# Kernel tuning notes

Measured on AMD Instinct MI355X. Metric: run time of the kernel, lower is better.

Reference implementation:

```python
import jax, jax.numpy as jnp
import numpy as np

B, PLEN, D = 32, 1024, 256


def setup_inputs() -> dict:
    key = jax.random.key(0)
    ks = jax.random.split(key, 8)
    u = lambda k, shape: jax.random.uniform(k, shape, jnp.float32, -0.05, 0.05)
    return {
        "P": jax.random.normal(ks[0], (B, PLEN, D), jnp.float32),
        "w_itr_att": u(ks[1], (3 * D,)),
        "w1": u(ks[2], (2 * D, D)),
        "w2": u(ks[3], (2 * D, D)),
        "w3": u(ks[4], (2 * D, D)),
        "b1": u(ks[5], (D,)),
        "b2": u(ks[6], (D,)),
        "b3": u(ks[7], (D,)),
    }


def reference(P, w_itr_att, w1, w2, w3, b1, b2, b3):
    d = P.shape[-1]
    # alpha(a,b) = w_itr_att . [a ; b ; a*b]; split w into the three d-chunks
    wa, wb, wc = w_itr_att[:d], w_itr_att[d:2 * d], w_itr_att[2 * d:]
    # pairwise score A[b,i,j] = wa.P_i + wb.P_j + wc.(P_i * P_j)
    sa = P @ wa                                   # (b, p)
    sb = P @ wb                                   # (b, p)
    A = sa[:, :, None] + sb[:, None, :] + jnp.einsum('bid,bjd->bij', P * wc, P)
    itr_attn = jnp.einsum('bij,bjd->bid', jax.nn.softmax(A, axis=2), P)
    cat = jnp.concatenate([P, itr_attn], axis=-1)  # (b, p, 2d)
    z = jnp.tanh(cat @ w1 + b1)
    r = jax.nn.sigmoid(cat @ w2 + b2)
    f = jax.nn.sigmoid(cat @ w3 + b3)
    return r * P + f * z
```

## Files before the change

kernel.cpp:

```cpp
#include <hip/hip_runtime.h>
#include <hip/hip_bf16.h>

typedef unsigned short u16;
typedef unsigned int   u32;

using bf16x8 = __attribute__((ext_vector_type(8))) short;
using f32x4  = __attribute__((ext_vector_type(4))) float;

#define NB 32
#define NP 1024
#define ND 256

__device__ __forceinline__ u16 f2bf(float x){
  u32 u = __float_as_uint(x);
  u += 0x7FFFu + ((u >> 16) & 1u);
  return (u16)(u >> 16);
}

__device__ __forceinline__ float bf2f(u16 x){
  return __uint_as_float((u32)x << 16);
}

__device__ __forceinline__ void glds16(const void* g, void* l){
  __builtin_amdgcn_global_load_lds((const __attribute__((address_space(1))) void*)g,
                                   (__attribute__((address_space(3))) void*)l, 16, 0, 0);
}

__global__ void prep_rows(const float* __restrict__ P, const float* __restrict__ wi,
                          u16* __restrict__ Pbf, float* __restrict__ sbv){
  const int row  = blockIdx.x * 4 + (threadIdx.x >> 6);
  const int lane = threadIdx.x & 63;
  const float4 p  = *(const float4*)(P  + (size_t)row * ND + lane * 4);
  const float4 wb = *(const float4*)(wi + ND + lane * 4);
  ushort4 pb;
  pb.x = f2bf(p.x); pb.y = f2bf(p.y); pb.z = f2bf(p.z); pb.w = f2bf(p.w);
  *(ushort4*)(Pbf + (size_t)row * ND + lane * 4) = pb;
  float s = p.x*wb.x + p.y*wb.y + p.z*wb.z + p.w*wb.w;
  #pragma unroll
  for (int m = 1; m < 64; m <<= 1) s += __shfl_xor(s, m, 64);
  if (lane == 0) sbv[row] = s;
}

__global__ void prep_w(const float* __restrict__ w1, const float* __restrict__ w2,
                       const float* __restrict__ w3, u16* __restrict__ Wp){
  const int t = blockIdx.x;
  const float* w = (t < 16) ? w1 : ((t < 32) ? w2 : w3);
  const int tid = threadIdx.x;
  #pragma unroll
  for (int j = 0; j < 4; ++j){
    int item = tid + 256 * j;
    int c = item >> 6, lane = item & 63;
    int ncol = ((t & 15) << 4) + (lane & 15);
    int k0 = 32 * c + 8 * (lane >> 4);
    u16 tmp[8];
    #pragma unroll
    for (int e = 0; e < 8; ++e) tmp[e] = f2bf(w[(size_t)(k0 + e) * 256 + ncol]);
    *(uint4*)(Wp + ((size_t)(t * 16 + c) * 64 + lane) * 8) = *(uint4*)tmp;
  }
}

__global__ void transpose_p(const u16* __restrict__ Pbf, u16* __restrict__ PbfT){
  const int b = blockIdx.z, jt = blockIdx.x, dt = blockIdx.y;
  __shared__ u16 T[64][72];
  const int tid = threadIdx.x;
  #pragma unroll
  for (int it = 0; it < 2; ++it){
    int cc = tid + 256 * it;
    int j = cc >> 3, c8 = cc & 7;
    uint4 v = *(const uint4*)(Pbf + ((size_t)b * NP + jt * 64 + j) * ND + dt * 64 + c8 * 8);
    *(uint4*)&T[j][c8 * 8] = v;
  }
  __syncthreads();
  #pragma unroll
  for (int it = 0; it < 2; ++it){
    int cc = tid + 256 * it;
    int d = cc >> 3, c8 = cc & 7;
    u16 tmp[8];
    #pragma unroll
    for (int k = 0; k < 8; ++k) tmp[k] = T[c8 * 8 + k][d];
    *(uint4*)(PbfT + ((size_t)b * ND + dt * 64 + d) * NP + jt * 64 + c8 * 8) = *(uint4*)tmp;
  }
}

__launch_bounds__(512, 1)
__global__ void attn_kernel(const float* __restrict__ P, const float* __restrict__ wi,
                            const u16* __restrict__ Pbf, const u16* __restrict__ PbfT,
                            const float* __restrict__ sbv, u16* __restrict__ attnb){
  const int p    = blockIdx.x;
  const int bid  = ((p & 7) << 5) | (p >> 3);
  const int b    = bid >> 3;
  const int q0   = (bid & 7) << 7;
  const int tid  = threadIdx.x;
  const int wave = tid >> 6, lane = tid & 63, lo = lane & 15, hi = lane >> 4;

  __shared__ __align__(16) u16 KtA[2][16384];
  __shared__ __align__(16) u16 VtA[2][16384];
  __shared__ __align__(16) u16 Sp[8][16][72];

  bf16x8 qf[8];
  {
    const int qrow = q0 + wave * 16 + lo;
    const float* prow = P  + ((size_t)b * NP + qrow) * ND;
    const float* wcp  = wi + 512;
    #pragma unroll
    for (int c = 0; c < 8; ++c){
      const int d0 = 32 * c + 8 * hi;
      float4 a  = *(const float4*)(prow + d0);
      float4 a2 = *(const float4*)(prow + d0 + 4);
      float4 wa  = *(const float4*)(wcp + d0);
      float4 wa2 = *(const float4*)(wcp + d0 + 4);
      bf16x8 q;
      q[0]=(short)f2bf(a.x*wa.x);  q[1]=(short)f2bf(a.y*wa.y);
      q[2]=(short)f2bf(a.z*wa.z);  q[3]=(short)f2bf(a.w*wa.w);
      q[4]=(short)f2bf(a2.x*wa2.x); q[5]=(short)f2bf(a2.y*wa2.y);
      q[6]=(short)f2bf(a2.z*wa2.z); q[7]=(short)f2bf(a2.w*wa2.w);
      qf[c] = q;
    }
  }

  f32x4 of[16];
  #pragma unroll
  for (int t = 0; t < 16; ++t) of[t] = (f32x4){0.f,0.f,0.f,0.f};
  float mx[4] = {-1e30f,-1e30f,-1e30f,-1e30f};
  float ls[4] = {0.f,0.f,0.f,0.f};

  const u16* kslab = Pbf  + (size_t)b * NP * ND;
  const u16* vslab = PbfT + (size_t)b * ND * NP;

  auto stageKV = [&](int kt, int buf){
    const int kbase = kt * 64;
    char* KtB = (char*)KtA[buf];
    char* VtB = (char*)VtA[buf];
    #pragma unroll
    for (int r = 0; r < 4; ++r){
      int off = r * 8192 + tid * 16;
      int ck  = off >> 10;
      int row = ((off >> 4) & 63) ^ ((ck & 1) << 4);
      glds16((const char*)(kslab + (size_t)(kbase + row) * ND + ck * 8), KtB + off);
    }
    #pragma unroll
    for (int r = 0; r < 4; ++r){
      int off = r * 8192 + tid * 16;
      int c   = off >> 12;
      int d   = ((off >> 4) & 255) ^ ((c & 1) << 4);
      glds16((const char*)(vslab + (size_t)d * NP + kbase + c * 8), VtB + off);
    }
  };

  float sbc[4], sbn[4];
  stageKV(0, 0);
  #pragma unroll
  for (int nt = 0; nt < 4; ++nt) sbc[nt] = sbv[(size_t)b * NP + nt * 16 + lo];
  __syncthreads();

  for (int kt = 0; kt < 16; ++kt){
    const int cur = kt & 1;
    if (kt < 15){
      stageKV(kt + 1, cur ^ 1);
      #pragma unroll
      for (int nt = 0; nt < 4; ++nt)
        sbn[nt] = sbv[(size_t)b * NP + (kt + 1) * 64 + nt * 16 + lo];
    }
    const char* KtB = (const char*)KtA[cur];
    const char* VtB = (const char*)VtA[cur];

    f32x4 s[4];
    #pragma unroll
    for (int nt = 0; nt < 4; ++nt){
      f32x4 acc = (f32x4){0.f,0.f,0.f,0.f};
      #pragma unroll
      for (int c = 0; c < 8; ++c){
        int ck = 4 * c + hi;
        int ad = ck * 1024 + ((((nt << 4) + lo) ^ ((ck & 1) << 4)) << 4);
        bf16x8 kf = *(const bf16x8*)(KtB + ad);
        acc = __builtin_amdgcn_mfma_f32_16x16x32_bf16(qf[c], kf, acc, 0, 0, 0);
      }
      s[nt] = acc;
      float sv = sbc[nt];
      #pragma unroll
      for (int r = 0; r < 4; ++r) s[nt][r] += sv;
    }

    float scale[4];
    #pragma unroll
    for (int r = 0; r < 4; ++r){
      float v = fmaxf(fmaxf(s[0][r], s[1][r]), fmaxf(s[2][r], s[3][r]));
      v = fmaxf(v, __shfl_xor(v, 1, 64));
      v = fmaxf(v, __shfl_xor(v, 2, 64));
      v = fmaxf(v, __shfl_xor(v, 4, 64));
      v = fmaxf(v, __shfl_xor(v, 8, 64));
      float mnew = fmaxf(mx[r], v);
      scale[r] = __expf(mx[r] - mnew);
      mx[r] = mnew;
      float rs = 0.f;
      #pragma unroll
      for (int nt = 0; nt < 4; ++nt){
        float pv = __expf(s[nt][r] - mnew);
        s[nt][r] = pv; rs += pv;
      }
      rs += __shfl_xor(rs, 1, 64);
      rs += __shfl_xor(rs, 2, 64);
      rs += __shfl_xor(rs, 4, 64);
      rs += __shfl_xor(rs, 8, 64);
      ls[r] = ls[r] * scale[r] + rs;
    }
    #pragma unroll
    for (int t = 0; t < 16; ++t){
      #pragma unroll
      for (int r = 0; r < 4; ++r) of[t][r] *= scale[r];
    }
    #pragma unroll
    for (int nt = 0; nt < 4; ++nt)
      #pragma unroll
      for (int r = 0; r < 4; ++r)
        Sp[wave][4 * hi + r][16 * nt + lo] = f2bf(s[nt][r]);

    #pragma unroll
    for (int kk = 0; kk < 2; ++kk){
      bf16x8 pa = *(const bf16x8*)&Sp[wave][lo][32 * kk + 8 * hi];
      int c = 4 * kk + hi;
      int cb = c * 4096, cs = (c & 1) << 4;
      #pragma unroll
      for (int t = 0; t < 16; ++t){
        int ad = cb + ((((t << 4) + lo) ^ cs) << 4);
        bf16x8 vb = *(const bf16x8*)(VtB + ad);
        of[t] = __builtin_amdgcn_mfma_f32_16x16x32_bf16(pa, vb, of[t], 0, 0, 0);
      }
    }
    sbc[0] = sbn[0]; sbc[1] = sbn[1]; sbc[2] = sbn[2]; sbc[3] = sbn[3];
    if (kt < 15) __syncthreads();
  }

  const int qrow = q0 + wave * 16;
  #pragma unroll
  for (int t = 0; t < 16; ++t){
    #pragma unroll
    for (int r = 0; r < 4; ++r){
      float o = of[t][r] / ls[r];
      attnb[((size_t)b * NP + qrow + 4 * hi + r) * ND + 16 * t + lo] = f2bf(o);
    }
  }
}

__launch_bounds__(256, 2)
__global__ void mlp_kernel(const u16* __restrict__ Pbf, const u16* __restrict__ attnb,
                           const u16* __restrict__ Wp,
                           const float* __restrict__ b1, const float* __restrict__ b2,
                           const float* __restrict__ b3, float* __restrict__ out){
  const int p    = blockIdx.x;
  const int swz  = ((p & 7) << 7) | (p >> 3);
  const int mt   = swz >> 2, cg = swz & 3;
  const int tid  = threadIdx.x;
  const int wave = tid >> 6, lane = tid & 63, lo = lane & 15, hi = lane >> 4;
  const int tq   = 4 * cg + wave;
  const int m0   = mt * 128;

  __shared__ __align__(16) u16 Ab[2][128 * 64];

  f32x4 acc[3][8];
  #pragma unroll
  for (int e = 0; e < 3; ++e)
    #pragma unroll
    for (int m = 0; m < 8; ++m) acc[e][m] = (f32x4){0.f,0.f,0.f,0.f};

  auto stage = [&](int s, int buf){
    const u16* xs = (s < 4) ? (Pbf   + (size_t)m0 * ND + s * 64)
                            : (attnb + (size_t)m0 * ND + (s - 4) * 64);
    char* dst = (char*)Ab[buf];
    #pragma unroll
    for (int it = 0; it < 4; ++it){
      int off = it * 4096 + wave * 1024 + lane * 16;
      int row = off >> 7;
      int cl  = (off & 127) ^ ((row & 7) << 4);
      glds16((const char*)(xs + (size_t)row * ND) + cl, dst + it * 4096 + wave * 1024);
    }
  };

  stage(0, 0);
  __syncthreads();

  for (int s = 0; s < 8; ++s){
    if (s < 7) stage(s + 1, (s + 1) & 1);
    const char* ab = (const char*)Ab[s & 1];
    #pragma unroll
    for (int cc = 0; cc < 2; ++cc){
      const int c = 2 * s + cc;
      bf16x8 wf[3];
      #pragma unroll
      for (int e = 0; e < 3; ++e)
        wf[e] = *(const bf16x8*)(Wp + ((size_t)((tq + 16 * e) * 16 + c) * 64 + lane) * 8);
      #pragma unroll
      for (int m = 0; m < 8; ++m){
        int row = 16 * m + lo;
        bf16x8 af = *(const bf16x8*)(ab + row * 128 + ((64 * cc + 16 * hi) ^ ((row & 7) << 4)));
        #pragma unroll
        for (int e = 0; e < 3; ++e)
          acc[e][m] = __builtin_amdgcn_mfma_f32_16x16x32_bf16(af, wf[e], acc[e][m], 0, 0, 0);
      }
    }
    __syncthreads();
  }

  const int d = 16 * tq + lo;
  const float bb1 = b1[d], bb2 = b2[d], bb3 = b3[d];
  #pragma unroll
  for (int m = 0; m < 8; ++m){
    #pragma unroll
    for (int r = 0; r < 4; ++r){
      const int row = m0 + 16 * m + 4 * hi + r;
      float y1 = acc[0][m][r] + bb1;
      float y2 = acc[1][m][r] + bb2;
      float y3 = acc[2][m][r] + bb3;
      float pv = bf2f(Pbf[(size_t)row * ND + d]);
      float e2 = __expf(2.f * y1);
      float z  = (e2 - 1.f) / (e2 + 1.f);
      float rr = 1.f / (1.f + __expf(-y2));
      float ff = 1.f / (1.f + __expf(-y3));
      out[(size_t)row * ND + d] = rr * pv + ff * z;
    }
  }
}

extern "C" void kernel_launch(void* const* d_in, const int* in_sizes, int n_in,
                              void* d_out, int out_size, void* d_ws, size_t ws_size,
                              hipStream_t stream){
  const float* P  = (const float*)d_in[0];
  const float* wi = (const float*)d_in[1];
  const float* w1 = (const float*)d_in[2];
  const float* w2 = (const float*)d_in[3];
  const float* w3 = (const float*)d_in[4];
  const float* b1 = (const float*)d_in[5];
  const float* b2 = (const float*)d_in[6];
  const float* b3 = (const float*)d_in[7];
  float* out = (float*)d_out;

  char* ws = (char*)d_ws;
  u16*   Pbf   = (u16*)  (ws);
  u16*   PbfT  = (u16*)  (ws + (16u << 20));
  u16*   attnb = (u16*)  (ws + (32u << 20));
  u16*   Wp    = (u16*)  (ws + (48u << 20));
  float* sbv   = (float*)(ws + (49u << 20));

  prep_rows<<<8192, 256, 0, stream>>>(P, wi, Pbf, sbv);
  prep_w<<<48, 256, 0, stream>>>(w1, w2, w3, Wp);
  transpose_p<<<dim3(16, 4, 32), 256, 0, stream>>>(Pbf, PbfT);
  attn_kernel<<<256, 512, 0, stream>>>(P, wi, Pbf, PbfT, sbv, attnb);
  mlp_kernel<<<1024, 256, 0, stream>>>(Pbf, attnb, Wp, b1, b2, b3, out);
}
```

Measured before the change: 133.0 us.

## Split attention into smaller blocks, shrink KV tile, and add lazy softmax rescale

The attention kernel now uses 256-thread blocks covering 64 query rows, launched as 512 blocks, with 32-key tiles over 32 iterations. Less LDS per block lets two blocks share a CU. The online softmax now skips the max update and rescale of the output accumulators unless some score exceeds the running max by more than 8, and the row-sum shuffle reduction moves out of the loop to the end. The MLP kernel's launch bounds ask for 4 waves per SIMD. The trade-offs are twice as many barriers and K/V loads per query, possible register spills under the tighter MLP bound, and exponentials up to e^8 held in bf16 when the rescale is skipped.

```diff
diff --git a/kernel.cpp b/kernel.cpp
--- a/kernel.cpp
+++ b/kernel.cpp
@@ -82,20 +82,20 @@
   }
 }
 
-__launch_bounds__(512, 1)
+__launch_bounds__(256, 2)
 __global__ void attn_kernel(const float* __restrict__ P, const float* __restrict__ wi,
                             const u16* __restrict__ Pbf, const u16* __restrict__ PbfT,
                             const float* __restrict__ sbv, u16* __restrict__ attnb){
   const int p    = blockIdx.x;
-  const int bid  = ((p & 7) << 5) | (p >> 3);
-  const int b    = bid >> 3;
-  const int q0   = (bid & 7) << 7;
+  const int bid  = ((p & 7) << 6) | (p >> 3);
+  const int b    = bid >> 4;
+  const int q0   = (bid & 15) << 6;
   const int tid  = threadIdx.x;
   const int wave = tid >> 6, lane = tid & 63, lo = lane & 15, hi = lane >> 4;
 
-  __shared__ __align__(16) u16 KtA[2][16384];
-  __shared__ __align__(16) u16 VtA[2][16384];
-  __shared__ __align__(16) u16 Sp[8][16][72];
+  __shared__ __align__(16) u16 KtA[2][8192];
+  __shared__ __align__(16) u16 VtA[2][8192];
+  __shared__ __align__(16) u16 Sp[4][16][40];
 
   bf16x8 qf[8];
   {
@@ -128,50 +128,50 @@
   const u16* vslab = PbfT + (size_t)b * ND * NP;
 
   auto stageKV = [&](int kt, int buf){
-    const int kbase = kt * 64;
+    const int kbase = kt * 32;
     char* KtB = (char*)KtA[buf];
     char* VtB = (char*)VtA[buf];
     #pragma unroll
     for (int r = 0; r < 4; ++r){
-      int off = r * 8192 + tid * 16;
-      int ck  = off >> 10;
-      int row = ((off >> 4) & 63) ^ ((ck & 1) << 4);
+      int off = r * 4096 + tid * 16;
+      int ck  = off >> 9;
+      int row = ((off >> 4) & 31) ^ ((ck & 1) << 4);
       glds16((const char*)(kslab + (size_t)(kbase + row) * ND + ck * 8), KtB + off);
     }
     #pragma unroll
     for (int r = 0; r < 4; ++r){
-      int off = r * 8192 + tid * 16;
+      int off = r * 4096 + tid * 16;
       int c   = off >> 12;
       int d   = ((off >> 4) & 255) ^ ((c & 1) << 4);
       glds16((const char*)(vslab + (size_t)d * NP + kbase + c * 8), VtB + off);
     }
   };
 
-  float sbc[4], sbn[4];
+  float sbc[2], sbn[2];
   stageKV(0, 0);
   #pragma unroll
-  for (int nt = 0; nt < 4; ++nt) sbc[nt] = sbv[(size_t)b * NP + nt * 16 + lo];
+  for (int nt = 0; nt < 2; ++nt) sbc[nt] = sbv[(size_t)b * NP + nt * 16 + lo];
   __syncthreads();
 
-  for (int kt = 0; kt < 16; ++kt){
+  for (int kt = 0; kt < 32; ++kt){
     const int cur = kt & 1;
-    if (kt < 15){
+    if (kt < 31){
       stageKV(kt + 1, cur ^ 1);
       #pragma unroll
-      for (int nt = 0; nt < 4; ++nt)
-        sbn[nt] = sbv[(size_t)b * NP + (kt + 1) * 64 + nt * 16 + lo];
+      for (int nt = 0; nt < 2; ++nt)
+        sbn[nt] = sbv[(size_t)b * NP + (kt + 1) * 32 + nt * 16 + lo];
     }
     const char* KtB = (const char*)KtA[cur];
     const char* VtB = (const char*)VtA[cur];
 
-    f32x4 s[4];
-    #pragma unroll
-    for (int nt = 0; nt < 4; ++nt){
+    f32x4 s[2];
+    #pragma unroll
+    for (int nt = 0; nt < 2; ++nt){
       f32x4 acc = (f32x4){0.f,0.f,0.f,0.f};
       #pragma unroll
       for (int c = 0; c < 8; ++c){
         int ck = 4 * c + hi;
-        int ad = ck * 1024 + ((((nt << 4) + lo) ^ ((ck & 1) << 4)) << 4);
+        int ad = ck * 512 + ((((nt << 4) + lo) ^ ((ck & 1) << 4)) << 4);
         bf16x8 kf = *(const bf16x8*)(KtB + ad);
         acc = __builtin_amdgcn_mfma_f32_16x16x32_bf16(qf[c], kf, acc, 0, 0, 0);
       }
@@ -181,56 +181,57 @@
       for (int r = 0; r < 4; ++r) s[nt][r] += sv;
     }
 
-    float scale[4];
-    #pragma unroll
-    for (int r = 0; r < 4; ++r){
-      float v = fmaxf(fmaxf(s[0][r], s[1][r]), fmaxf(s[2][r], s[3][r]));
-      v = fmaxf(v, __shfl_xor(v, 1, 64));
-      v = fmaxf(v, __shfl_xor(v, 2, 64));
-      v = fmaxf(v, __shfl_xor(v, 4, 64));
-      v = fmaxf(v, __shfl_xor(v, 8, 64));
-      float mnew = fmaxf(mx[r], v);
-      scale[r] = __expf(mx[r] - mnew);
-      mx[r] = mnew;
-      float rs = 0.f;
-      #pragma unroll
-      for (int nt = 0; nt < 4; ++nt){
-        float pv = __expf(s[nt][r] - mnew);
-        s[nt][r] = pv; rs += pv;
+    float md = -1e30f;
+    #pragma unroll
+    for (int nt = 0; nt < 2; ++nt)
+      #pragma unroll
+      for (int r = 0; r < 4; ++r) md = fmaxf(md, s[nt][r] - mx[r]);
+    if (!__all(md <= 8.f)){
+      float scale[4];
+      #pragma unroll
+      for (int r = 0; r < 4; ++r){
+        float v = fmaxf(s[0][r], s[1][r]);
+        v = fmaxf(v, __shfl_xor(v, 1, 64));
+        v = fmaxf(v, __shfl_xor(v, 2, 64));
+        v = fmaxf(v, __shfl_xor(v, 4, 64));
+        v = fmaxf(v, __shfl_xor(v, 8, 64));
+        float mnew = fmaxf(mx[r], v);
+        scale[r] = __expf(mx[r] - mnew);
+        mx[r] = mnew;
+        ls[r] *= scale[r];
       }
-      rs += __shfl_xor(rs, 1, 64);
-      rs += __shfl_xor(rs, 2, 64);
-      rs += __shfl_xor(rs, 4, 64);
-      rs += __shfl_xor(rs, 8, 64);
-      ls[r] = ls[r] * scale[r] + rs;
-    }
+      #pragma unroll
+      for (int t = 0; t < 16; ++t)
+        #pragma unroll
+        for (int r = 0; r < 4; ++r) of[t][r] *= scale[r];
+    }
+    #pragma unroll
+    for (int nt = 0; nt < 2; ++nt)
+      #pragma unroll
+      for (int r = 0; r < 4; ++r){
+        float pv = __expf(s[nt][r] - mx[r]);
+        ls[r] += pv;
+        Sp[wave][4 * hi + r][16 * nt + lo] = f2bf(pv);
+      }
+
+    bf16x8 pa = *(const bf16x8*)&Sp[wave][lo][8 * hi];
     #pragma unroll
     for (int t = 0; t < 16; ++t){
-      #pragma unroll
-      for (int r = 0; r < 4; ++r) of[t][r] *= scale[r];
-    }
-    #pragma unroll
-    for (int nt = 0; nt < 4; ++nt)
-      #pragma unroll
-      for (int r = 0; r < 4; ++r)
-        Sp[wave][4 * hi + r][16 * nt + lo] = f2bf(s[nt][r]);
-
-    #pragma unroll
-    for (int kk = 0; kk < 2; ++kk){
-      bf16x8 pa = *(const bf16x8*)&Sp[wave][lo][32 * kk + 8 * hi];
-      int c = 4 * kk + hi;
-      int cb = c * 4096, cs = (c & 1) << 4;
-      #pragma unroll
-      for (int t = 0; t < 16; ++t){
-        int ad = cb + ((((t << 4) + lo) ^ cs) << 4);
-        bf16x8 vb = *(const bf16x8*)(VtB + ad);
-        of[t] = __builtin_amdgcn_mfma_f32_16x16x32_bf16(pa, vb, of[t], 0, 0, 0);
-      }
-    }
-    sbc[0] = sbn[0]; sbc[1] = sbn[1]; sbc[2] = sbn[2]; sbc[3] = sbn[3];
-    if (kt < 15) __syncthreads();
-  }
-
+      int ad = hi * 4096 + ((((t << 4) + lo) ^ ((hi & 1) << 4)) << 4);
+      bf16x8 vb = *(const bf16x8*)(VtB + ad);
+      of[t] = __builtin_amdgcn_mfma_f32_16x16x32_bf16(pa, vb, of[t], 0, 0, 0);
+    }
+    sbc[0] = sbn[0]; sbc[1] = sbn[1];
+    if (kt < 31) __syncthreads();
+  }
+
+  #pragma unroll
+  for (int r = 0; r < 4; ++r){
+    ls[r] += __shfl_xor(ls[r], 1, 64);
+    ls[r] += __shfl_xor(ls[r], 2, 64);
+    ls[r] += __shfl_xor(ls[r], 4, 64);
+    ls[r] += __shfl_xor(ls[r], 8, 64);
+  }
   const int qrow = q0 + wave * 16;
   #pragma unroll
   for (int t = 0; t < 16; ++t){
@@ -242,7 +243,7 @@
   }
 }
 
-__launch_bounds__(256, 2)
+__launch_bounds__(256, 4)
 __global__ void mlp_kernel(const u16* __restrict__ Pbf, const u16* __restrict__ attnb,
                            const u16* __restrict__ Wp,
                            const float* __restrict__ b1, const float* __restrict__ b2,
@@ -344,6 +345,6 @@
   prep_rows<<<8192, 256, 0, stream>>>(P, wi, Pbf, sbv);
   prep_w<<<48, 256, 0, stream>>>(w1, w2, w3, Wp);
   transpose_p<<<dim3(16, 4, 32), 256, 0, stream>>>(Pbf, PbfT);
-  attn_kernel<<<256, 512, 0, stream>>>(P, wi, Pbf, PbfT, sbv, attnb);
+  attn_kernel<<<512, 256, 0, stream>>>(P, wi, Pbf, PbfT, sbv, attnb);
   mlp_kernel<<<1024, 256, 0, stream>>>(Pbf, attnb, Wp, b1, b2, b3, out);
 }
```

Result: slower. 202.8 us (+52.5%).
